# Optimization experiments

Hardware: AMD Instinct MI355X
Metric: run time of the kernel (lower is better)

Reference implementation:

```python
import jax, jax.numpy as jnp
import numpy as np

D_DEPTH = 41   # arange(4.0, 45.0, 1.0)
CAM_C = 64
IMG_H, IMG_W = 512, 1408
DOWNS = 16
FH, FW = IMG_H // DOWNS, IMG_W // DOWNS  # 32, 88
NX, NY, NZ = 200, 200, 1                 # gen_dx_bx of the fixed bounds
DX = np.array([0.25, 0.25, 20.0], np.float32)
BX = np.array([-25.0 + 0.125, 0.0 + 0.125, 0.0], np.float32)  # row0 + row2/2


def _frustum():
    # [D, FH, FW, 3] with (pixel_x, pixel_y, depth)
    ds = np.arange(4.0, 45.0, 1.0, dtype=np.float32).reshape(-1, 1, 1)
    xs = np.linspace(0, IMG_W - 1, FW, dtype=np.float32).reshape(1, 1, FW)
    ys = np.linspace(0, IMG_H - 1, FH, dtype=np.float32).reshape(1, FH, 1)
    ds, xs, ys = np.broadcast_arrays(
        np.broadcast_to(ds, (D_DEPTH, FH, FW)), xs, ys)[0:1] + list(
        np.broadcast_arrays(xs, ys, ds)[:2]) if False else (
        np.broadcast_to(ds, (D_DEPTH, FH, FW)),
        np.broadcast_to(xs, (D_DEPTH, FH, FW)),
        np.broadcast_to(ys, (D_DEPTH, FH, FW)))
    return np.stack([xs, ys, ds], axis=-1)


def setup_inputs() -> dict:
    key = jax.random.key(0)
    k1, k2, k3 = jax.random.split(key, 3)
    B = 4
    feat = jax.random.normal(k1, (B, 256, FH, FW), jnp.float32)
    # realistic pinhole intrinsics with per-sample focal jitter
    fx = 0.5 * IMG_W / np.tan(np.deg2rad(35.0))
    s = 0.9 + 0.2 * jax.random.uniform(k2, (B,), jnp.float32)
    intrins = (jnp.zeros((B, 3, 3), jnp.float32)
               .at[:, 0, 0].set(fx * s)
               .at[:, 1, 1].set(fx * s)
               .at[:, 0, 2].set(IMG_W / 2.0)
               .at[:, 1, 2].set(IMG_H / 2.0)
               .at[:, 2, 2].set(1.0))
    w_depth = jax.random.normal(k3, (D_DEPTH + CAM_C, 256), jnp.float32) * 0.05
    b_depth = jnp.zeros((D_DEPTH + CAM_C,), jnp.float32)
    return {"feat": feat, "intrins": intrins, "w_depth": w_depth, "b_depth": b_depth}


def reference(feat, intrins, w_depth, b_depth):
    B = feat.shape[0]
    # depthnet 1x1 conv: 256 -> D + C
    x = jnp.einsum('bchw,oc->bohw', feat, w_depth) + b_depth[None, :, None, None]
    depth = jax.nn.softmax(x[:, :D_DEPTH], axis=1)               # [B,D,fH,fW]
    # lift: depth distribution outer-product with context features
    lifted = depth[:, None] * x[:, D_DEPTH:, None]               # [B,C,D,fH,fW]
    feats = lifted.transpose(0, 2, 3, 4, 1).reshape(-1, CAM_C)   # [B*D*fH*fW, C]

    # geometry: unproject frustum pixels through inverse intrinsics
    fr = jnp.asarray(_frustum())                                 # [D,fH,fW,3]
    pix = jnp.concatenate([fr[..., :2] * fr[..., 2:3], fr[..., 2:3]], axis=-1)
    inv = jnp.linalg.inv(intrins)                                # [B,3,3]
    pts = jnp.einsum('bij,dhwj->bdhwi', inv, pix)                # [B,D,fH,fW,3]

    dx = jnp.asarray(DX); bx = jnp.asarray(BX)
    geom = ((pts - (bx - dx / 2.0)) / dx).astype(jnp.int32)      # trunc like .long()
    geom = geom.reshape(-1, 3)
    n_per = geom.shape[0] // B
    bix = jnp.repeat(jnp.arange(B, dtype=jnp.int32), n_per)
    gx, gy, gz = geom[:, 0], geom[:, 1], geom[:, 2]
    kept = ((gx >= 0) & (gx < NX) & (gy >= 0) & (gy < NY)
            & (gz >= 0) & (gz < NZ))
    ranks = gx * (NY * NZ * B) + gy * (NZ * B) + gz * B + bix
    nseg = NX * NY * NZ * B
    seg = jnp.where(kept, ranks, nseg)  # out-of-range -> dummy bucket
    # sort+cumsum+diff dedup over ranks == segment sum per voxel
    sums = jax.ops.segment_sum(feats, seg, num_segments=nseg + 1)[:nseg]
    grid = sums.reshape(NX, NY, NZ, B, CAM_C).transpose(3, 4, 2, 0, 1)  # B,C,Z,X,Y
    bev = grid.reshape(B, CAM_C * NZ, NX, NY)  # cat of Z slices along channels
    return bev[:, :, :196, :]
```

## Files before the change

kernel.cpp:

```cpp
#include <hip/hip_runtime.h>
#include <math.h>

#define B_      4
#define CIN     256
#define FH_     32
#define FW_     88
#define HWN     (FH_*FW_)
#define DND     41
#define CC      64
#define NO      105
#define NXg     200
#define NYg     200
#define NXOUT   196
#define PLANE   (NXOUT*NYg)
#define XPAD    112
#define NPOS    (B_*HWN)

#define GX0     71
#define GXW     58
#define GYW     29
#define WCELLS  (GXW*GYW)
#define WSG_F   (B_*WCELLS*CC)

__global__ void zero_ws_kernel(float4* __restrict__ p) {
  int i = blockIdx.x*blockDim.x + threadIdx.x;
  if (i < WSG_F/4) p[i] = make_float4(0.f,0.f,0.f,0.f);
}

__global__ __launch_bounds__(256) void gemm_kernel(
    const float* __restrict__ feat, const float* __restrict__ wd,
    const float* __restrict__ bd, float* __restrict__ xbuf)
{
  __shared__ float __attribute__((aligned(16))) ft[64*64];
  __shared__ float __attribute__((aligned(16))) Wl[64*68];

  const int t     = threadIdx.x;
  const int mtile = blockIdx.x;
  const int o0    = blockIdx.y * 64;
  const int b     = mtile / 44;
  const int hw0   = (mtile - b*44) * 64;
  const float* featB = feat + (size_t)b*CIN*HWN + hw0;

  const int tm = t & 15;
  const int to = t >> 4;
  float acc[4][4] = {{0,0,0,0},{0,0,0,0},{0,0,0,0},{0,0,0,0}};

  for (int k0 = 0; k0 < CIN; k0 += 64) {
    #pragma unroll
    for (int r = 0; r < 4; ++r) {
      int idx = r*256 + t;
      int c = idx >> 4, m4 = (idx & 15) * 4;
      *reinterpret_cast<float4*>(&ft[c*64 + m4]) =
        *reinterpret_cast<const float4*>(&featB[(size_t)(k0+c)*HWN + m4]);
    }
    #pragma unroll
    for (int r = 0; r < 4; ++r) {
      int idx = r*256 + t;
      int o = idx >> 4, c4 = (idx & 15) * 4;
      int og = o0 + o;
      float4 v = make_float4(0.f,0.f,0.f,0.f);
      if (og < NO) v = *reinterpret_cast<const float4*>(&wd[(size_t)og*CIN + k0 + c4]);
      *reinterpret_cast<float4*>(&Wl[o*68 + c4]) = v;
    }
    __syncthreads();
    #pragma unroll 8
    for (int c = 0; c < 64; ++c) {
      float4 fm = *reinterpret_cast<const float4*>(&ft[c*64 + tm*4]);
      float w0v = Wl[(to*4+0)*68 + c];
      float w1v = Wl[(to*4+1)*68 + c];
      float w2v = Wl[(to*4+2)*68 + c];
      float w3v = Wl[(to*4+3)*68 + c];
      acc[0][0] += fm.x*w0v; acc[0][1] += fm.x*w1v; acc[0][2] += fm.x*w2v; acc[0][3] += fm.x*w3v;
      acc[1][0] += fm.y*w0v; acc[1][1] += fm.y*w1v; acc[1][2] += fm.y*w2v; acc[1][3] += fm.y*w3v;
      acc[2][0] += fm.z*w0v; acc[2][1] += fm.z*w1v; acc[2][2] += fm.z*w2v; acc[2][3] += fm.z*w3v;
      acc[3][0] += fm.w*w0v; acc[3][1] += fm.w*w1v; acc[3][2] += fm.w*w2v; acc[3][3] += fm.w*w3v;
    }
    __syncthreads();
  }

  const int obase = o0 + to*4;
  float bv[4];
  #pragma unroll
  for (int j = 0; j < 4; ++j) bv[j] = (obase + j < NO) ? bd[obase + j] : 0.f;
  const int pos0 = mtile*64 + tm*4;
  #pragma unroll
  for (int i = 0; i < 4; ++i) {
    int pos = pos0 + i;
    float* row = xbuf + (size_t)pos*XPAD + obase;
    if (obase + 3 < NO) {
      float4 v = make_float4(acc[i][0]+bv[0], acc[i][1]+bv[1], acc[i][2]+bv[2], acc[i][3]+bv[3]);
      *reinterpret_cast<float4*>(row) = v;
    } else {
      #pragma unroll
      for (int j = 0; j < 4; ++j)
        if (obase + j < NO) row[j] = acc[i][j] + bv[j];
    }
  }
}

__global__ __launch_bounds__(256) void scatter_kernel(
    const float* __restrict__ xbuf, const float* __restrict__ intr,
    float* __restrict__ wsg)
{
  const int t    = threadIdx.x;
  const int lane = t & 63;
  const int pos  = blockIdx.x*4 + (t >> 6);
  const int b    = pos / HWN;
  const int rem  = pos - b*HWN;
  const int h    = rem / FW_;
  const int w    = rem - h*FW_;

  const float fv  = intr[b*9 + 0];
  const float cxv = intr[b*9 + 2];
  const float cyv = intr[b*9 + 5];
  const float rf  = __fdiv_rn(1.0f, fv);
  const float i02 = -__fmul_rn(rf, cxv);
  const float i12 = -__fmul_rn(rf, cyv);

  const float xw = (float)((double)w * (1407.0/87.0));
  const float yh = (float)((double)h * (511.0/31.0));

  int cells[6];
  bool any = false;
  #pragma unroll
  for (int d = 0; d < 6; ++d) {
    float dval = 4.0f + (float)d;
    float px = __fadd_rn(__fmul_rn(rf, __fmul_rn(xw, dval)), __fmul_rn(i02, dval));
    float py = __fadd_rn(__fmul_rn(rf, __fmul_rn(yh, dval)), __fmul_rn(i12, dval));
    int gx = (int)__fdiv_rn(__fadd_rn(px, 25.0f), 0.25f);
    int gy = (int)__fdiv_rn(py, 0.25f);
    int c = -1;
    if (gx >= 0 && gx < NXOUT && gy >= 0 && gy < NYg) {
      int gxw = gx - GX0;
      if (gxw >= 0 && gxw < GXW && gy < GYW) c = gxw*GYW + gy;
    }
    cells[d] = c;
    any = any || (c >= 0);
  }
  if (!any) return;

  const float* xr = xbuf + (size_t)pos*XPAD;
  float logit = (lane < DND) ? xr[lane] : -1e30f;
  float mx = logit;
  #pragma unroll
  for (int s = 1; s < 64; s <<= 1) mx = fmaxf(mx, __shfl_xor(mx, s));
  float e = (lane < DND) ? expf(logit - mx) : 0.f;
  float den = e;
  #pragma unroll
  for (int s = 1; s < 64; s <<= 1) den += __shfl_xor(den, s);
  const float rden = 1.0f / den;

  const float xc = xr[DND + lane];
  float* wsB = wsg + (size_t)b*WCELLS*CC;

  int curCell = -2; float wacc = 0.f;
  #pragma unroll
  for (int d = 0; d < 6; ++d) {
    int cd = cells[d];
    float pd = __shfl(e, d) * rden;
    if (cd != curCell) {
      if (curCell >= 0) atomicAdd(wsB + (size_t)curCell*CC + lane, wacc * xc);
      curCell = cd; wacc = 0.f;
    }
    if (cd >= 0) wacc += pd;
  }
  if (curCell >= 0) atomicAdd(wsB + (size_t)curCell*CC + lane, wacc * xc);
}

__global__ void transpose_kernel(const float* __restrict__ wsg, float* __restrict__ out) {
  int tid = blockIdx.x*blockDim.x + threadIdx.x;
  if (tid >= B_*CC*NXOUT*(NYg/4)) return;
  int gy4 = tid % (NYg/4);
  int r   = tid / (NYg/4);
  int gx  = r % NXOUT; r /= NXOUT;
  int c   = r % CC;
  int b   = r / CC;
  float4 v = make_float4(0.f,0.f,0.f,0.f);
  int gxw = gx - GX0;
  int gy0 = gy4*4;
  if (gxw >= 0 && gxw < GXW && gy0 < GYW) {
    const float* base = wsg + ((size_t)((b*GXW + gxw)*GYW))*CC + c;
    v.x = base[(size_t)(gy0+0)*CC];
    if (gy0+1 < GYW) v.y = base[(size_t)(gy0+1)*CC];
    if (gy0+2 < GYW) v.z = base[(size_t)(gy0+2)*CC];
    if (gy0+3 < GYW) v.w = base[(size_t)(gy0+3)*CC];
  }
  reinterpret_cast<float4*>(out)[tid] = v;
}

extern "C" void kernel_launch(void* const* d_in, const int* in_sizes, int n_in,
                              void* d_out, int out_size, void* d_ws, size_t ws_size,
                              hipStream_t stream) {
  const float* feat = (const float*)d_in[0];
  const float* intr = (const float*)d_in[1];
  const float* wd   = (const float*)d_in[2];
  const float* bd   = (const float*)d_in[3];
  float* out  = (float*)d_out;
  float* xbuf = (float*)d_ws;
  float* wsg  = (float*)d_ws + (size_t)NPOS*XPAD;

  zero_ws_kernel<<<dim3((WSG_F/4 + 255)/256), dim3(256), 0, stream>>>((float4*)wsg);
  gemm_kernel<<<dim3(176, 2), dim3(256), 0, stream>>>(feat, wd, bd, xbuf);
  scatter_kernel<<<dim3(NPOS/4), dim3(256), 0, stream>>>(xbuf, intr, wsg);
  transpose_kernel<<<dim3(B_*CC*NXOUT*(NYg/4)/256), dim3(256), 0, stream>>>(wsg, out);
}
```

Baseline: 116.9 us.

## Halve GEMM M-tile and transpose weight tile in shared memory

Shrinks the GEMM position tile from 64 to 32, doubling the grid to 704 blocks so the device's many CUs are better filled. The weight tile is now stored transposed in LDS so each thread reads its four output weights with a single float4 load instead of four scalar loads. The trade-off is half the arithmetic per LDS load of features and more blocks re-reading the weights, plus scalar strided LDS stores during the transpose.

Result: faster. 114.2 us (-2.3%).

```diff
diff --git a/kernel.cpp b/kernel.cpp
--- a/kernel.cpp
+++ b/kernel.cpp
@@ -27,53 +27,54 @@
   if (i < WSG_F/4) p[i] = make_float4(0.f,0.f,0.f,0.f);
 }
 
+#define BM 32
+#define KCH 64
+#define LDO 68
 __global__ __launch_bounds__(256) void gemm_kernel(
     const float* __restrict__ feat, const float* __restrict__ wd,
     const float* __restrict__ bd, float* __restrict__ xbuf)
 {
-  __shared__ float __attribute__((aligned(16))) ft[64*64];
-  __shared__ float __attribute__((aligned(16))) Wl[64*68];
+  __shared__ float __attribute__((aligned(16))) ft[KCH*BM];
+  __shared__ float __attribute__((aligned(16))) Wl[KCH*LDO];
 
   const int t     = threadIdx.x;
   const int mtile = blockIdx.x;
   const int o0    = blockIdx.y * 64;
-  const int b     = mtile / 44;
-  const int hw0   = (mtile - b*44) * 64;
+  const int b     = mtile / 88;
+  const int hw0   = (mtile - b*88) * BM;
   const float* featB = feat + (size_t)b*CIN*HWN + hw0;
 
   const int tm = t & 15;
   const int to = t >> 4;
-  float acc[4][4] = {{0,0,0,0},{0,0,0,0},{0,0,0,0},{0,0,0,0}};
-
-  for (int k0 = 0; k0 < CIN; k0 += 64) {
+  float acc[2][4] = {{0,0,0,0},{0,0,0,0}};
+
+  for (int k0 = 0; k0 < CIN; k0 += KCH) {
     #pragma unroll
-    for (int r = 0; r < 4; ++r) {
+    for (int r = 0; r < 2; ++r) {
       int idx = r*256 + t;
-      int c = idx >> 4, m4 = (idx & 15) * 4;
-      *reinterpret_cast<float4*>(&ft[c*64 + m4]) =
+      int c = idx >> 3, m4 = (idx & 7) * 4;
+      *reinterpret_cast<float4*>(&ft[c*BM + m4]) =
         *reinterpret_cast<const float4*>(&featB[(size_t)(k0+c)*HWN + m4]);
     }
     #pragma unroll
-    for (int r = 0; r < 4; ++r) {
-      int idx = r*256 + t;
-      int o = idx >> 4, c4 = (idx & 15) * 4;
+    for (int pass = 0; pass < 4; ++pass) {
+      int o  = t & 63;
+      int c4 = ((t >> 6) + pass*4) * 4;
       int og = o0 + o;
       float4 v = make_float4(0.f,0.f,0.f,0.f);
       if (og < NO) v = *reinterpret_cast<const float4*>(&wd[(size_t)og*CIN + k0 + c4]);
-      *reinterpret_cast<float4*>(&Wl[o*68 + c4]) = v;
+      Wl[(c4+0)*LDO + o] = v.x;
+      Wl[(c4+1)*LDO + o] = v.y;
+      Wl[(c4+2)*LDO + o] = v.z;
+      Wl[(c4+3)*LDO + o] = v.w;
     }
     __syncthreads();
     #pragma unroll 8
-    for (int c = 0; c < 64; ++c) {
-      float4 fm = *reinterpret_cast<const float4*>(&ft[c*64 + tm*4]);
-      float w0v = Wl[(to*4+0)*68 + c];
-      float w1v = Wl[(to*4+1)*68 + c];
-      float w2v = Wl[(to*4+2)*68 + c];
-      float w3v = Wl[(to*4+3)*68 + c];
-      acc[0][0] += fm.x*w0v; acc[0][1] += fm.x*w1v; acc[0][2] += fm.x*w2v; acc[0][3] += fm.x*w3v;
-      acc[1][0] += fm.y*w0v; acc[1][1] += fm.y*w1v; acc[1][2] += fm.y*w2v; acc[1][3] += fm.y*w3v;
-      acc[2][0] += fm.z*w0v; acc[2][1] += fm.z*w1v; acc[2][2] += fm.z*w2v; acc[2][3] += fm.z*w3v;
-      acc[3][0] += fm.w*w0v; acc[3][1] += fm.w*w1v; acc[3][2] += fm.w*w2v; acc[3][3] += fm.w*w3v;
+    for (int c = 0; c < KCH; ++c) {
+      float2 fm = *reinterpret_cast<const float2*>(&ft[c*BM + tm*2]);
+      float4 wv = *reinterpret_cast<const float4*>(&Wl[c*LDO + to*4]);
+      acc[0][0] += fm.x*wv.x; acc[0][1] += fm.x*wv.y; acc[0][2] += fm.x*wv.z; acc[0][3] += fm.x*wv.w;
+      acc[1][0] += fm.y*wv.x; acc[1][1] += fm.y*wv.y; acc[1][2] += fm.y*wv.z; acc[1][3] += fm.y*wv.w;
     }
     __syncthreads();
   }
@@ -82,9 +83,9 @@
   float bv[4];
   #pragma unroll
   for (int j = 0; j < 4; ++j) bv[j] = (obase + j < NO) ? bd[obase + j] : 0.f;
-  const int pos0 = mtile*64 + tm*4;
-  #pragma unroll
-  for (int i = 0; i < 4; ++i) {
+  const int pos0 = mtile*BM + tm*2;
+  #pragma unroll
+  for (int i = 0; i < 2; ++i) {
     int pos = pos0 + i;
     float* row = xbuf + (size_t)pos*XPAD + obase;
     if (obase + 3 < NO) {
@@ -200,7 +201,7 @@
   float* wsg  = (float*)d_ws + (size_t)NPOS*XPAD;
 
   zero_ws_kernel<<<dim3((WSG_F/4 + 255)/256), dim3(256), 0, stream>>>((float4*)wsg);
-  gemm_kernel<<<dim3(176, 2), dim3(256), 0, stream>>>(feat, wd, bd, xbuf);
+  gemm_kernel<<<dim3(352, 2), dim3(256), 0, stream>>>(feat, wd, bd, xbuf);
   scatter_kernel<<<dim3(NPOS/4), dim3(256), 0, stream>>>(xbuf, intr, wsg);
   transpose_kernel<<<dim3(B_*CC*NXOUT*(NYg/4)/256), dim3(256), 0, stream>>>(wsg, out);
 }
```
